# Performance work log

Hardware: AMD Instinct MI355X
Metric: run time of the kernel (lower is better)

## Reference

```python
import jax, jax.numpy as jnp
import numpy as np

B, C_IN, N = 64, 1, 8192
WIDTH, MODES, NLAYERS = 64, 16, 4


def setup_inputs() -> dict:
    key = jax.random.key(0)
    ks = jax.random.split(key, 10)
    scale = 1.0 / (WIDTH * WIDTH)
    inp = {
        "x": jax.random.normal(ks[0], (B, C_IN, N), dtype=jnp.float32),
        # lifting p: Linear(2, width)
        "p_w": jax.random.normal(ks[1], (WIDTH, 2), dtype=jnp.float32) * 0.5,
        "p_b": jax.random.normal(ks[2], (WIDTH,), dtype=jnp.float32) * 0.1,
        # 4 spectral conv weights, complex stored as real/imag (uniform like torch.rand cfloat)
        "sc_wr": scale * jax.random.uniform(ks[3], (NLAYERS, WIDTH, WIDTH, MODES), dtype=jnp.float32),
        "sc_wi": scale * jax.random.uniform(ks[4], (NLAYERS, WIDTH, WIDTH, MODES), dtype=jnp.float32),
        # 4 pointwise (1x1) conv weights/biases
        "w_w": jax.random.normal(ks[5], (NLAYERS, WIDTH, WIDTH), dtype=jnp.float32) / np.sqrt(WIDTH),
        "w_b": jax.random.normal(ks[6], (NLAYERS, WIDTH), dtype=jnp.float32) * 0.1,
        # projection q: Linear(width, 1)
        "q_w": jax.random.normal(ks[7], (1, WIDTH), dtype=jnp.float32) / np.sqrt(WIDTH),
        "q_b": jax.random.normal(ks[8], (1,), dtype=jnp.float32) * 0.1,
    }
    return inp


def spectral_conv(x, wr, wi, n):
    # x: [b, i, n] real; weights complex [i, o, modes]
    x_ft = jnp.fft.rfft(x, axis=-1)                      # [b, i, n//2+1] complex
    w = (wr + 1j * wi).astype(jnp.complex64)
    out_modes = jnp.einsum('bix,iox->box', x_ft[:, :, :MODES], w)
    out_ft = jnp.zeros((x.shape[0], w.shape[1], n // 2 + 1), dtype=jnp.complex64)
    out_ft = out_ft.at[:, :, :MODES].set(out_modes)
    return jnp.fft.irfft(out_ft, n=n, axis=-1)


def reference(x, p_w, p_b, sc_wr, sc_wi, w_w, w_b, q_w, q_b):
    b, _, n = x.shape
    grid = jnp.broadcast_to(jnp.linspace(0.0, 1.0, n, dtype=jnp.float32)[None, None, :], (b, 1, n))
    h = jnp.concatenate([x, grid], axis=1)               # [b, 2, n]
    # lifting: Linear over channel dim
    h = jnp.einsum('bcn,wc->bwn', h, p_w) + p_b[None, :, None]
    for l in range(NLAYERS):
        x1 = spectral_conv(h, sc_wr[l], sc_wi[l], n)
        x2 = jnp.einsum('bin,oi->bon', h, w_w[l]) + w_b[l][None, :, None]
        h = jax.nn.gelu(x1 + x2, approximate=False)
    out = jnp.einsum('bwn,ow->bon', h, q_w) + q_b[None, :, None]  # [b, 1, n]
    return out
```

## Files before the change

kernel.cpp:

```cpp
#include <hip/hip_runtime.h>
#include <math.h>


typedef _Float16 f16;
typedef _Float16 f16x2 __attribute__((ext_vector_type(2)));
typedef _Float16 f16x4 __attribute__((ext_vector_type(4)));
typedef _Float16 f16x8 __attribute__((ext_vector_type(8)));
typedef float    f32x2 __attribute__((ext_vector_type(2)));
typedef float    f32x4 __attribute__((ext_vector_type(4)));
typedef unsigned int u32;

#define BB 64
#define NN 8192

#define HT_S 64
#define HO_S 136
#define WS_S 72
#define MS_S 40
#define BI_S 40
#define BF_S 136

__device__ __forceinline__ int ht_swz(int n) { return ((n & 7) ^ ((n >> 3) & 7)) << 3; }

__device__ __forceinline__ float gelu_f(float v) {
    float x  = v * 0.70710678118654752f;
    float ax = fabsf(x);
    float t  = __builtin_amdgcn_rcpf(fmaf(0.3275911f, ax, 1.0f));
    float p  = fmaf(1.061405429f, t, -1.453152027f);
    p = fmaf(p, t, 1.421413741f);
    p = fmaf(p, t, -0.284496736f);
    p = fmaf(p, t, 0.254829592f);
    p = p * t;
    float e  = __expf(-x * x);
    float er = fmaf(-p, e, 1.0f);
    er = copysignf(er, x);
    return 0.5f * fmaf(v, er, v);
}

__global__ __launch_bounds__(256) void fill_basis(f16* __restrict__ basF,
                                                  f16* __restrict__ basI,
                                                  const float* __restrict__ w_w,
                                                  f16* __restrict__ Wh,
                                                  float* __restrict__ Sz) {
    int n = blockIdx.x * 256 + threadIdx.x;
    f16 row[32];
#pragma unroll
    for (int k = 0; k < 16; ++k) {
        float s, c;
        sincospif((float)(k * n) * (1.0f / 4096.0f), &s, &c);
        basF[k * NN + n]        = (f16)c;
        basF[(16 + k) * NN + n] = (f16)(-s);
        row[2 * k]     = (f16)c;
        row[2 * k + 1] = (f16)s;
    }
#pragma unroll
    for (int q = 0; q < 4; ++q) *(f16x8*)&basI[n * 32 + 8 * q] = *(f16x8*)&row[8 * q];
    Wh[n]        = (f16)w_w[n];
    Wh[n + 8192] = (f16)w_w[n + 8192];
    f32x4* S4 = (f32x4*)Sz;
    f32x4 z = {0.f, 0.f, 0.f, 0.f};
#pragma unroll
    for (int u = 0; u < 4; ++u) S4[n * 4 + u] = z;
}

__global__ __launch_bounds__(1024) void mode_mix(float* __restrict__ S,
                                                 const float* __restrict__ wr,
                                                 const float* __restrict__ wi,
                                                 f16* __restrict__ Mph) {
    int b = blockIdx.x, t = threadIdx.x;
    __shared__ float Ss[32 * 66];
    if (t < 512) {
        f32x4 v = *(const f32x4*)&S[b * 2048 + t * 4];
        int rw = t >> 4, cl = (t & 15) * 4;
#pragma unroll
        for (int e = 0; e < 4; ++e) Ss[rw * 66 + cl + e] = v[e];
    }
    __syncthreads();
    *(f32x2*)&S[b * 2048 + t * 2] = (f32x2){0.f, 0.f};

    int o = t >> 4, k = t & 15;
    const float* wrp = wr + o * 16 + k;
    const float* wip = wi + o * 16 + k;
    float ar = 0.f, ai = 0.f;
#pragma unroll 8
    for (int i = 0; i < 64; ++i) {
        float sr = Ss[k * 66 + i], si = Ss[(16 + k) * 66 + i];
        float wrv = wrp[i * 1024];
        float wiv = wip[i * 1024];
        ar = fmaf(sr, wrv, ar); ar = fmaf(-si, wiv, ar);
        ai = fmaf(sr, wiv, ai); ai = fmaf(si, wrv, ai);
    }
    float sc = (k == 0 ? 1.0f : 2.0f) * (1.0f / 8192.0f);
    f16x2 outv = { (f16)(sc * ar), (f16)(-sc * ai) };
    *(f16x2*)&Mph[b * 2048 + o * 32 + 2 * k] = outv;
}

__device__ __forceinline__ void dft_epilogue(const f16* Hout, const f16* BasF,
                                             float* __restrict__ S, int b,
                                             int lane, int wv) {
    int q = lane >> 4, l15 = lane & 15;
    f32x4 sacc[2] = {{0.f,0.f,0.f,0.f},{0.f,0.f,0.f,0.f}};
#pragma unroll
    for (int ks = 0; ks < 4; ++ks) {
        int o = (wv << 4) + l15;
        f16x8 bh = *(const f16x8*)&Hout[o * HO_S + ks * 32 + q * 8];
#pragma unroll
        for (int mt = 0; mt < 2; ++mt) {
            f16x8 af = *(const f16x8*)&BasF[(mt * 16 + l15) * BF_S + ks * 32 + q * 8];
            sacc[mt] = __builtin_amdgcn_mfma_f32_16x16x32_f16(af, bh, sacc[mt], 0, 0, 0);
        }
    }
#pragma unroll
    for (int mt = 0; mt < 2; ++mt)
#pragma unroll
        for (int r = 0; r < 4; ++r)
            atomicAdd(&S[(b * 32 + mt * 16 + q * 4 + r) * 64 + (wv << 4) + l15],
                      sacc[mt][r]);
}

__global__ __launch_bounds__(256, 3) void lift_kernel(const float* __restrict__ x,
                                                      const float* __restrict__ p_w,
                                                      const float* __restrict__ p_b,
                                                      f16* __restrict__ h,
                                                      const f16* __restrict__ basF_g,
                                                      float* __restrict__ S) {
    __shared__ f16 Hout[64 * HO_S];
    __shared__ f16 BasF[32 * BF_S];
    int t = threadIdx.x;
    int b = blockIdx.x >> 6;
    int n0 = (blockIdx.x & 63) << 7;
#pragma unroll
    for (int r = 0; r < 4; ++r) {
        int o = (t >> 4) + 16 * r;
        int ns = (t & 15) << 3;
        float w0 = p_w[2 * o], w1 = p_w[2 * o + 1], pb = p_b[o];
        f16 vals[8];
#pragma unroll
        for (int j = 0; j < 8; ++j) {
            int n = n0 + ns + j;
            float xv = x[(b << 13) + n];
            vals[j] = (f16)(w0 * xv + w1 * ((float)n * (1.0f / 8191.0f)) + pb);
        }
        *(f16x8*)&Hout[o * HO_S + ns] = *(f16x8*)vals;
        *(f16x8*)(h + (((size_t)(b * 64 + o)) << 13) + n0 + ns) = *(f16x8*)vals;
    }
#pragma unroll
    for (int u = 0; u < 2; ++u) {
        int km = t >> 3, nn = (t & 7) * 16 + u * 8;
        *(f16x8*)&BasF[km * BF_S + nn] = *(const f16x8*)&basF_g[km * NN + n0 + nn];
    }
    __syncthreads();
    dft_epilogue(Hout, BasF, S, b, t & 63, t >> 6);
}

template <int DO_DFT>
__global__ __launch_bounds__(256, 3) void layer_kernel(f16* __restrict__ h,
                                                       const f16* __restrict__ Wl_h,
                                                       const float* __restrict__ bl,
                                                       const f16* __restrict__ Mph,
                                                       const f16* __restrict__ basF_g,
                                                       const f16* __restrict__ basI_g,
                                                       float* __restrict__ S,
                                                       const float* __restrict__ q_w,
                                                       const float* __restrict__ q_b,
                                                       float* __restrict__ out) {
    __shared__ __align__(16) char pool[16384 + 9216];
    f16* Ht   = (f16*)pool;
    f16* Ws   = (f16*)(pool + 16384);
    f16* Hout = (f16*)pool;
    __shared__ f16 Ms2[64 * MS_S];
    __shared__ f16 BasI[128 * BI_S];
    __shared__ f16 BasF[32 * BF_S];
    __shared__ float bls[64];
    int t = threadIdx.x;
    int b = blockIdx.x >> 6;
    int n0 = (blockIdx.x & 63) << 7;
    f16* hb = h + (((size_t)(b * 64)) << 13) + n0;

    if (t < 128) {
        int ig = t >> 4, nb = t & 15;
        int i0 = ig << 3, ns = nb << 3;
        f16x8 R[8];
#pragma unroll
        for (int k = 0; k < 8; ++k)
            R[k] = *(const f16x8*)(hb + ((size_t)(i0 + k) << 13) + ns);
        const u32* rd = (const u32*)R;
        int swz = nb & 7;
#pragma unroll
        for (int j = 0; j < 8; ++j) {
            u32 o[4] __attribute__((aligned(16)));
            u32 sel = (j & 1) ? 0x07060302u : 0x05040100u;
            int jd = j >> 1;
#pragma unroll
            for (int e = 0; e < 4; ++e)
                o[e] = __builtin_amdgcn_perm(rd[(2 * e + 1) * 4 + jd],
                                             rd[(2 * e) * 4 + jd], sel);
            int col = i0 ^ ((j ^ swz) << 3);
            *(f16x8*)&Ht[(ns + j) * HT_S + col] = *(const f16x8*)o;
        }
    } else {
        int t2 = t - 128;
        {
            int o = t2 & 63, hs = (t2 >> 6) * 32;
            const f16* src = Wl_h + o * 64 + hs;
            f16* dst = &Ws[o * WS_S + hs];
#pragma unroll
            for (int u = 0; u < 4; ++u) *(f16x8*)&dst[8 * u] = *(const f16x8*)&src[8 * u];
        }
        {
            int o = t2 >> 1, seg = (t2 & 1) * 16;
            const f16* src = Mph + b * 2048 + o * 32 + seg;
            f16* dst = &Ms2[o * MS_S + seg];
            *(f16x8*)&dst[0] = *(const f16x8*)&src[0];
            *(f16x8*)&dst[8] = *(const f16x8*)&src[8];
        }
        {
            const f16* src = basI_g + (size_t)(n0 + t2) * 32;
            f16* dst = &BasI[t2 * BI_S];
#pragma unroll
            for (int u = 0; u < 4; ++u) *(f16x8*)&dst[8 * u] = *(const f16x8*)&src[8 * u];
        }
        if (DO_DFT) {
            int km = t2 >> 2, seg = (t2 & 3) * 32;
            const f16* src = basF_g + km * NN + n0 + seg;
            f16* dst = &BasF[km * BF_S + seg];
#pragma unroll
            for (int u = 0; u < 4; ++u) *(f16x8*)&dst[8 * u] = *(const f16x8*)&src[8 * u];
        }
    }
    if (t < 64) bls[t] = bl[t];
    __syncthreads();

    int lane = t & 63, wv = t >> 6;
    int q = lane >> 4, l15 = lane & 15;

    f16x8 Bw[4][2], Bm[4];
#pragma unroll
    for (int ct = 0; ct < 4; ++ct) {
#pragma unroll
        for (int ks = 0; ks < 2; ++ks)
            Bw[ct][ks] = *(const f16x8*)&Ws[(ct * 16 + l15) * WS_S + ks * 32 + q * 8];
        Bm[ct] = *(const f16x8*)&Ms2[(ct * 16 + l15) * MS_S + q * 8];
    }

    f32x4 acc[4][2];
#pragma unroll
    for (int ct = 0; ct < 4; ++ct)
#pragma unroll
        for (int m = 0; m < 2; ++m) acc[ct][m] = (f32x4){0.f, 0.f, 0.f, 0.f};

#pragma unroll
    for (int mtl = 0; mtl < 2; ++mtl) {
        int nrow = (2 * wv + mtl) * 16 + l15;
        const f16* hrow = &Ht[nrow * HT_S];
        int g3 = ht_swz(nrow);
#pragma unroll
        for (int ks = 0; ks < 2; ++ks) {
            f16x8 Ah = *(const f16x8*)&hrow[(ks * 32 + q * 8) ^ g3];
#pragma unroll
            for (int ct = 0; ct < 4; ++ct)
                acc[ct][mtl] = __builtin_amdgcn_mfma_f32_16x16x32_f16(
                    Ah, Bw[ct][ks], acc[ct][mtl], 0, 0, 0);
        }
        f16x8 Ab = *(const f16x8*)&BasI[nrow * BI_S + q * 8];
#pragma unroll
        for (int ct = 0; ct < 4; ++ct)
            acc[ct][mtl] = __builtin_amdgcn_mfma_f32_16x16x32_f16(
                Ab, Bm[ct], acc[ct][mtl], 0, 0, 0);
    }

    float bv[4];
#pragma unroll
    for (int ct = 0; ct < 4; ++ct) bv[ct] = bls[ct * 16 + l15];
    __syncthreads();
#pragma unroll
    for (int ct = 0; ct < 4; ++ct) {
        int o = ct * 16 + l15;
#pragma unroll
        for (int mtl = 0; mtl < 2; ++mtl) {
            int nbase = (2 * wv + mtl) * 16 + q * 4;
            float g[4];
#pragma unroll
            for (int r = 0; r < 4; ++r)
                g[r] = gelu_f(acc[ct][mtl][r] + bv[ct]);
            f16x2 lo = __builtin_bit_cast(f16x2, __builtin_amdgcn_cvt_pkrtz(g[0], g[1]));
            f16x2 hi = __builtin_bit_cast(f16x2, __builtin_amdgcn_cvt_pkrtz(g[2], g[3]));
            f16x4 pk = {lo[0], lo[1], hi[0], hi[1]};
            *(f16x4*)&Hout[o * HO_S + nbase] = pk;
        }
    }
    __syncthreads();

    if (DO_DFT) {
        dft_epilogue(Hout, BasF, S, b, lane, wv);
#pragma unroll
        for (int r = 0; r < 4; ++r) {
            int o = (t >> 4) + 16 * r;
            int ns = (t & 15) << 3;
            *(f16x8*)(hb + ((size_t)o << 13) + ns) = *(f16x8*)&Hout[o * HO_S + ns];
        }
    } else {
        if (t < 128) {
            int n = t;
            float s = q_b[0];
#pragma unroll 8
            for (int o = 0; o < 64; ++o) s += q_w[o] * (float)Hout[o * HO_S + n];
            out[(b << 13) + n0 + n] = s;
        }
    }
}

extern "C" void kernel_launch(void* const* d_in, const int* in_sizes, int n_in,
                              void* d_out, int out_size, void* d_ws, size_t ws_size,
                              hipStream_t stream) {
    const float* x     = (const float*)d_in[0];
    const float* p_w   = (const float*)d_in[1];
    const float* p_b   = (const float*)d_in[2];
    const float* sc_wr = (const float*)d_in[3];
    const float* sc_wi = (const float*)d_in[4];
    const float* w_w   = (const float*)d_in[5];
    const float* w_b   = (const float*)d_in[6];
    const float* q_w   = (const float*)d_in[7];
    const float* q_b   = (const float*)d_in[8];
    float* out = (float*)d_out;

    char* ws = (char*)d_ws;
    f16*   h    = (f16*)ws;
    float* S    = (float*)(ws + 67108864ull);
    f16*   Mph  = (f16*)(ws + 67633152ull);
    f16*   basF = (f16*)(ws + 67895296ull);
    f16*   basI = (f16*)(ws + 68419584ull);
    f16*   Wh   = (f16*)(ws + 68943872ull);

    hipLaunchKernelGGL(fill_basis, dim3(NN / 256), dim3(256), 0, stream,
                       basF, basI, w_w, Wh, S);
    hipLaunchKernelGGL(lift_kernel, dim3(BB * 64), dim3(256), 0, stream,
                       x, p_w, p_b, h, basF, S);
    for (int l = 0; l < 4; ++l) {
        hipLaunchKernelGGL(mode_mix, dim3(BB), dim3(1024), 0, stream,
                           S, sc_wr + l * 65536, sc_wi + l * 65536, Mph);
        if (l < 3) {
            hipLaunchKernelGGL((layer_kernel<1>), dim3(BB * 64), dim3(256), 0, stream,
                               h, Wh + l * 4096, w_b + l * 64, Mph, basF, basI, S,
                               q_w, q_b, out);
        } else {
            hipLaunchKernelGGL((layer_kernel<0>), dim3(BB * 64), dim3(256), 0, stream,
                               h, Wh + l * 4096, w_b + l * 64, Mph, basF, basI, S,
                               q_w, q_b, out);
        }
    }
}
```

Baseline: 277.5 us.

## Split forward DFT into a standalone kernel and process two tiles per layer block

The per-tile DFT epilogue with global float atomics is moved into a dedicated dft_kernel that reads h from global memory and reduces across waves in shared memory, so S no longer needs zeroing or atomics. Layer blocks now handle two 128-column tiles each, loading weights once and raising the occupancy hint. The final layer folds the q projection into registers with shuffle reductions instead of staging in LDS. The trade-off is an extra kernel launch and an extra full read of h per layer in exchange for removing atomic contention and the BasF staging.

```diff
diff --git a/kernel.cpp b/kernel.cpp
--- a/kernel.cpp
+++ b/kernel.cpp
@@ -6,7 +6,6 @@
 typedef _Float16 f16x2 __attribute__((ext_vector_type(2)));
 typedef _Float16 f16x4 __attribute__((ext_vector_type(4)));
 typedef _Float16 f16x8 __attribute__((ext_vector_type(8)));
-typedef float    f32x2 __attribute__((ext_vector_type(2)));
 typedef float    f32x4 __attribute__((ext_vector_type(4)));
 typedef unsigned int u32;
 
@@ -16,9 +15,8 @@
 #define HT_S 64
 #define HO_S 136
 #define WS_S 72
-#define MS_S 40
+#define MS_S 32
 #define BI_S 40
-#define BF_S 136
 
 __device__ __forceinline__ int ht_swz(int n) { return ((n & 7) ^ ((n >> 3) & 7)) << 3; }
 
@@ -40,8 +38,7 @@
 __global__ __launch_bounds__(256) void fill_basis(f16* __restrict__ basF,
                                                   f16* __restrict__ basI,
                                                   const float* __restrict__ w_w,
-                                                  f16* __restrict__ Wh,
-                                                  float* __restrict__ Sz) {
+                                                  f16* __restrict__ Wh) {
     int n = blockIdx.x * 256 + threadIdx.x;
     f16 row[32];
 #pragma unroll
@@ -57,13 +54,71 @@
     for (int q = 0; q < 4; ++q) *(f16x8*)&basI[n * 32 + 8 * q] = *(f16x8*)&row[8 * q];
     Wh[n]        = (f16)w_w[n];
     Wh[n + 8192] = (f16)w_w[n + 8192];
-    f32x4* S4 = (f32x4*)Sz;
-    f32x4 z = {0.f, 0.f, 0.f, 0.f};
-#pragma unroll
-    for (int u = 0; u < 4; ++u) S4[n * 4 + u] = z;
-}
-
-__global__ __launch_bounds__(1024) void mode_mix(float* __restrict__ S,
+}
+
+__global__ __launch_bounds__(256) void lift_kernel(const float* __restrict__ x,
+                                                   const float* __restrict__ p_w,
+                                                   const float* __restrict__ p_b,
+                                                   f16* __restrict__ h) {
+    int t = threadIdx.x;
+    int b = blockIdx.x >> 6;
+    int n0 = (blockIdx.x & 63) << 7;
+    int ns = (t & 15) << 3;
+    f32x4 X0 = *(const f32x4*)&x[(b << 13) + n0 + ns];
+    f32x4 X1 = *(const f32x4*)&x[(b << 13) + n0 + ns + 4];
+#pragma unroll
+    for (int r = 0; r < 4; ++r) {
+        int o = (t >> 4) + 16 * r;
+        float w0 = p_w[2 * o], w1 = p_w[2 * o + 1], pb = p_b[o];
+        f16 vals[8];
+#pragma unroll
+        for (int j = 0; j < 8; ++j) {
+            int n = n0 + ns + j;
+            float xv = (j < 4) ? X0[j] : X1[j - 4];
+            vals[j] = (f16)(w0 * xv + w1 * ((float)n * (1.0f / 8191.0f)) + pb);
+        }
+        *(f16x8*)(h + (((size_t)(b * 64 + o)) << 13) + n0 + ns) = *(f16x8*)vals;
+    }
+}
+
+__global__ __launch_bounds__(512) void dft_kernel(const f16* __restrict__ h,
+                                                  const f16* __restrict__ basF,
+                                                  float* __restrict__ S) {
+    __shared__ float Sp[8 * 512];
+    int b = blockIdx.x >> 2, ct = blockIdx.x & 3;
+    int t = threadIdx.x;
+    int wv = t >> 6, lane = t & 63;
+    int q = lane >> 4, l15 = lane & 15;
+
+    const f16* hrow = h + (((size_t)(b * 64 + ct * 16 + l15)) << 13);
+    const f16* a0 = basF + (size_t)l15 * NN;
+    const f16* a1 = basF + (size_t)(16 + l15) * NN;
+    int kb0 = (wv << 10) + (q << 3);
+
+    f32x4 acc0 = {0.f, 0.f, 0.f, 0.f}, acc1 = {0.f, 0.f, 0.f, 0.f};
+#pragma unroll 4
+    for (int kk = 0; kk < 32; ++kk) {
+        int kb = kb0 + (kk << 5);
+        f16x8 Bv = *(const f16x8*)&hrow[kb];
+        f16x8 A0 = *(const f16x8*)&a0[kb];
+        f16x8 A1 = *(const f16x8*)&a1[kb];
+        acc0 = __builtin_amdgcn_mfma_f32_16x16x32_f16(A0, Bv, acc0, 0, 0, 0);
+        acc1 = __builtin_amdgcn_mfma_f32_16x16x32_f16(A1, Bv, acc1, 0, 0, 0);
+    }
+#pragma unroll
+    for (int r = 0; r < 4; ++r) {
+        Sp[wv * 512 + (q * 4 + r) * 16 + l15]       = acc0[r];
+        Sp[wv * 512 + (16 + q * 4 + r) * 16 + l15]  = acc1[r];
+    }
+    __syncthreads();
+    float s = 0.f;
+#pragma unroll
+    for (int w = 0; w < 8; ++w) s += Sp[w * 512 + t];
+    int km = t >> 4, il = t & 15;
+    S[(b * 32 + km) * 64 + ct * 16 + il] = s;
+}
+
+__global__ __launch_bounds__(1024) void mode_mix(const float* __restrict__ S,
                                                  const float* __restrict__ wr,
                                                  const float* __restrict__ wi,
                                                  f16* __restrict__ Mph) {
@@ -76,8 +131,6 @@
         for (int e = 0; e < 4; ++e) Ss[rw * 66 + cl + e] = v[e];
     }
     __syncthreads();
-    *(f32x2*)&S[b * 2048 + t * 2] = (f32x2){0.f, 0.f};
-
     int o = t >> 4, k = t & 15;
     const float* wrp = wr + o * 16 + k;
     const float* wip = wi + o * 16 + k;
@@ -95,72 +148,12 @@
     *(f16x2*)&Mph[b * 2048 + o * 32 + 2 * k] = outv;
 }
 
-__device__ __forceinline__ void dft_epilogue(const f16* Hout, const f16* BasF,
-                                             float* __restrict__ S, int b,
-                                             int lane, int wv) {
-    int q = lane >> 4, l15 = lane & 15;
-    f32x4 sacc[2] = {{0.f,0.f,0.f,0.f},{0.f,0.f,0.f,0.f}};
-#pragma unroll
-    for (int ks = 0; ks < 4; ++ks) {
-        int o = (wv << 4) + l15;
-        f16x8 bh = *(const f16x8*)&Hout[o * HO_S + ks * 32 + q * 8];
-#pragma unroll
-        for (int mt = 0; mt < 2; ++mt) {
-            f16x8 af = *(const f16x8*)&BasF[(mt * 16 + l15) * BF_S + ks * 32 + q * 8];
-            sacc[mt] = __builtin_amdgcn_mfma_f32_16x16x32_f16(af, bh, sacc[mt], 0, 0, 0);
-        }
-    }
-#pragma unroll
-    for (int mt = 0; mt < 2; ++mt)
-#pragma unroll
-        for (int r = 0; r < 4; ++r)
-            atomicAdd(&S[(b * 32 + mt * 16 + q * 4 + r) * 64 + (wv << 4) + l15],
-                      sacc[mt][r]);
-}
-
-__global__ __launch_bounds__(256, 3) void lift_kernel(const float* __restrict__ x,
-                                                      const float* __restrict__ p_w,
-                                                      const float* __restrict__ p_b,
-                                                      f16* __restrict__ h,
-                                                      const f16* __restrict__ basF_g,
-                                                      float* __restrict__ S) {
-    __shared__ f16 Hout[64 * HO_S];
-    __shared__ f16 BasF[32 * BF_S];
-    int t = threadIdx.x;
-    int b = blockIdx.x >> 6;
-    int n0 = (blockIdx.x & 63) << 7;
-#pragma unroll
-    for (int r = 0; r < 4; ++r) {
-        int o = (t >> 4) + 16 * r;
-        int ns = (t & 15) << 3;
-        float w0 = p_w[2 * o], w1 = p_w[2 * o + 1], pb = p_b[o];
-        f16 vals[8];
-#pragma unroll
-        for (int j = 0; j < 8; ++j) {
-            int n = n0 + ns + j;
-            float xv = x[(b << 13) + n];
-            vals[j] = (f16)(w0 * xv + w1 * ((float)n * (1.0f / 8191.0f)) + pb);
-        }
-        *(f16x8*)&Hout[o * HO_S + ns] = *(f16x8*)vals;
-        *(f16x8*)(h + (((size_t)(b * 64 + o)) << 13) + n0 + ns) = *(f16x8*)vals;
-    }
-#pragma unroll
-    for (int u = 0; u < 2; ++u) {
-        int km = t >> 3, nn = (t & 7) * 16 + u * 8;
-        *(f16x8*)&BasF[km * BF_S + nn] = *(const f16x8*)&basF_g[km * NN + n0 + nn];
-    }
-    __syncthreads();
-    dft_epilogue(Hout, BasF, S, b, t & 63, t >> 6);
-}
-
-template <int DO_DFT>
-__global__ __launch_bounds__(256, 3) void layer_kernel(f16* __restrict__ h,
+template <int PROJ>
+__global__ __launch_bounds__(256, 4) void layer_kernel(f16* __restrict__ h,
                                                        const f16* __restrict__ Wl_h,
                                                        const float* __restrict__ bl,
                                                        const f16* __restrict__ Mph,
-                                                       const f16* __restrict__ basF_g,
                                                        const f16* __restrict__ basI_g,
-                                                       float* __restrict__ S,
                                                        const float* __restrict__ q_w,
                                                        const float* __restrict__ q_b,
                                                        float* __restrict__ out) {
@@ -170,35 +163,14 @@
     f16* Hout = (f16*)pool;
     __shared__ f16 Ms2[64 * MS_S];
     __shared__ f16 BasI[128 * BI_S];
-    __shared__ f16 BasF[32 * BF_S];
-    __shared__ float bls[64];
     int t = threadIdx.x;
-    int b = blockIdx.x >> 6;
-    int n0 = (blockIdx.x & 63) << 7;
-    f16* hb = h + (((size_t)(b * 64)) << 13) + n0;
-
-    if (t < 128) {
-        int ig = t >> 4, nb = t & 15;
-        int i0 = ig << 3, ns = nb << 3;
-        f16x8 R[8];
-#pragma unroll
-        for (int k = 0; k < 8; ++k)
-            R[k] = *(const f16x8*)(hb + ((size_t)(i0 + k) << 13) + ns);
-        const u32* rd = (const u32*)R;
-        int swz = nb & 7;
-#pragma unroll
-        for (int j = 0; j < 8; ++j) {
-            u32 o[4] __attribute__((aligned(16)));
-            u32 sel = (j & 1) ? 0x07060302u : 0x05040100u;
-            int jd = j >> 1;
-#pragma unroll
-            for (int e = 0; e < 4; ++e)
-                o[e] = __builtin_amdgcn_perm(rd[(2 * e + 1) * 4 + jd],
-                                             rd[(2 * e) * 4 + jd], sel);
-            int col = i0 ^ ((j ^ swz) << 3);
-            *(f16x8*)&Ht[(ns + j) * HT_S + col] = *(const f16x8*)o;
-        }
-    } else {
+    int b = blockIdx.x >> 5;
+    int g = blockIdx.x & 31;
+    f16* hbase = h + (((size_t)(b * 64)) << 13);
+    int lane = t & 63, wv = t >> 6;
+    int q = lane >> 4, l15 = lane & 15;
+
+    if (t >= 128) {
         int t2 = t - 128;
         {
             int o = t2 & 63, hs = (t2 >> 6) * 32;
@@ -214,99 +186,135 @@
             *(f16x8*)&dst[0] = *(const f16x8*)&src[0];
             *(f16x8*)&dst[8] = *(const f16x8*)&src[8];
         }
-        {
+    }
+    float bv[4];
+#pragma unroll
+    for (int ct = 0; ct < 4; ++ct) bv[ct] = bl[ct * 16 + l15];
+
+    f16x8 Bw[4][2], Bm[4];
+
+    for (int tile = 0; tile < 2; ++tile) {
+        int n0 = ((g << 1) + tile) << 7;
+        f16* hbt = hbase + n0;
+
+        if (t < 128) {
+            int ig = t >> 4, nb = t & 15;
+            int i0 = ig << 3, ns = nb << 3;
+            f16x8 R[8];
+#pragma unroll
+            for (int k = 0; k < 8; ++k)
+                R[k] = *(const f16x8*)(hbt + ((size_t)(i0 + k) << 13) + ns);
+            const u32* rd = (const u32*)R;
+            int swz = nb & 7;
+#pragma unroll
+            for (int j = 0; j < 8; ++j) {
+                u32 o[4] __attribute__((aligned(16)));
+                u32 sel = (j & 1) ? 0x07060302u : 0x05040100u;
+                int jd = j >> 1;
+#pragma unroll
+                for (int e = 0; e < 4; ++e)
+                    o[e] = __builtin_amdgcn_perm(rd[(2 * e + 1) * 4 + jd],
+                                                 rd[(2 * e) * 4 + jd], sel);
+                int col = i0 ^ ((j ^ swz) << 3);
+                *(f16x8*)&Ht[(ns + j) * HT_S + col] = *(const f16x8*)o;
+            }
+        } else {
+            int t2 = t - 128;
             const f16* src = basI_g + (size_t)(n0 + t2) * 32;
             f16* dst = &BasI[t2 * BI_S];
 #pragma unroll
             for (int u = 0; u < 4; ++u) *(f16x8*)&dst[8 * u] = *(const f16x8*)&src[8 * u];
         }
-        if (DO_DFT) {
-            int km = t2 >> 2, seg = (t2 & 3) * 32;
-            const f16* src = basF_g + km * NN + n0 + seg;
-            f16* dst = &BasF[km * BF_S + seg];
-#pragma unroll
-            for (int u = 0; u < 4; ++u) *(f16x8*)&dst[8 * u] = *(const f16x8*)&src[8 * u];
-        }
-    }
-    if (t < 64) bls[t] = bl[t];
-    __syncthreads();
-
-    int lane = t & 63, wv = t >> 6;
-    int q = lane >> 4, l15 = lane & 15;
-
-    f16x8 Bw[4][2], Bm[4];
-#pragma unroll
-    for (int ct = 0; ct < 4; ++ct) {
-#pragma unroll
-        for (int ks = 0; ks < 2; ++ks)
-            Bw[ct][ks] = *(const f16x8*)&Ws[(ct * 16 + l15) * WS_S + ks * 32 + q * 8];
-        Bm[ct] = *(const f16x8*)&Ms2[(ct * 16 + l15) * MS_S + q * 8];
-    }
-
-    f32x4 acc[4][2];
-#pragma unroll
-    for (int ct = 0; ct < 4; ++ct)
-#pragma unroll
-        for (int m = 0; m < 2; ++m) acc[ct][m] = (f32x4){0.f, 0.f, 0.f, 0.f};
-
-#pragma unroll
-    for (int mtl = 0; mtl < 2; ++mtl) {
-        int nrow = (2 * wv + mtl) * 16 + l15;
-        const f16* hrow = &Ht[nrow * HT_S];
-        int g3 = ht_swz(nrow);
-#pragma unroll
-        for (int ks = 0; ks < 2; ++ks) {
-            f16x8 Ah = *(const f16x8*)&hrow[(ks * 32 + q * 8) ^ g3];
+        __syncthreads();
+
+        if (tile == 0) {
+#pragma unroll
+            for (int ct = 0; ct < 4; ++ct) {
+#pragma unroll
+                for (int ks = 0; ks < 2; ++ks)
+                    Bw[ct][ks] = *(const f16x8*)&Ws[(ct * 16 + l15) * WS_S + ks * 32 + q * 8];
+                Bm[ct] = *(const f16x8*)&Ms2[(ct * 16 + l15) * MS_S + q * 8];
+            }
+        }
+
+        f32x4 acc[4][2];
+#pragma unroll
+        for (int ct = 0; ct < 4; ++ct)
+#pragma unroll
+            for (int m = 0; m < 2; ++m) acc[ct][m] = (f32x4){0.f, 0.f, 0.f, 0.f};
+
+#pragma unroll
+        for (int mtl = 0; mtl < 2; ++mtl) {
+            int nrow = (2 * wv + mtl) * 16 + l15;
+            const f16* hrow = &Ht[nrow * HT_S];
+            int g3 = ht_swz(nrow);
+#pragma unroll
+            for (int ks = 0; ks < 2; ++ks) {
+                f16x8 Ah = *(const f16x8*)&hrow[(ks * 32 + q * 8) ^ g3];
+#pragma unroll
+                for (int ct = 0; ct < 4; ++ct)
+                    acc[ct][mtl] = __builtin_amdgcn_mfma_f32_16x16x32_f16(
+                        Ah, Bw[ct][ks], acc[ct][mtl], 0, 0, 0);
+            }
+            f16x8 Ab = *(const f16x8*)&BasI[nrow * BI_S + q * 8];
 #pragma unroll
             for (int ct = 0; ct < 4; ++ct)
                 acc[ct][mtl] = __builtin_amdgcn_mfma_f32_16x16x32_f16(
-                    Ah, Bw[ct][ks], acc[ct][mtl], 0, 0, 0);
-        }
-        f16x8 Ab = *(const f16x8*)&BasI[nrow * BI_S + q * 8];
-#pragma unroll
-        for (int ct = 0; ct < 4; ++ct)
-            acc[ct][mtl] = __builtin_amdgcn_mfma_f32_16x16x32_f16(
-                Ab, Bm[ct], acc[ct][mtl], 0, 0, 0);
-    }
-
-    float bv[4];
-#pragma unroll
-    for (int ct = 0; ct < 4; ++ct) bv[ct] = bls[ct * 16 + l15];
-    __syncthreads();
-#pragma unroll
-    for (int ct = 0; ct < 4; ++ct) {
-        int o = ct * 16 + l15;
-#pragma unroll
-        for (int mtl = 0; mtl < 2; ++mtl) {
-            int nbase = (2 * wv + mtl) * 16 + q * 4;
-            float g[4];
-#pragma unroll
-            for (int r = 0; r < 4; ++r)
-                g[r] = gelu_f(acc[ct][mtl][r] + bv[ct]);
-            f16x2 lo = __builtin_bit_cast(f16x2, __builtin_amdgcn_cvt_pkrtz(g[0], g[1]));
-            f16x2 hi = __builtin_bit_cast(f16x2, __builtin_amdgcn_cvt_pkrtz(g[2], g[3]));
-            f16x4 pk = {lo[0], lo[1], hi[0], hi[1]};
-            *(f16x4*)&Hout[o * HO_S + nbase] = pk;
-        }
-    }
-    __syncthreads();
-
-    if (DO_DFT) {
-        dft_epilogue(Hout, BasF, S, b, lane, wv);
-#pragma unroll
-        for (int r = 0; r < 4; ++r) {
-            int o = (t >> 4) + 16 * r;
-            int ns = (t & 15) << 3;
-            *(f16x8*)(hb + ((size_t)o << 13) + ns) = *(f16x8*)&Hout[o * HO_S + ns];
-        }
-    } else {
-        if (t < 128) {
-            int n = t;
-            float s = q_b[0];
-#pragma unroll 8
-            for (int o = 0; o < 64; ++o) s += q_w[o] * (float)Hout[o * HO_S + n];
-            out[(b << 13) + n0 + n] = s;
-        }
+                    Ab, Bm[ct], acc[ct][mtl], 0, 0, 0);
+        }
+
+        if (!PROJ) {
+            __syncthreads();
+#pragma unroll
+            for (int ct = 0; ct < 4; ++ct) {
+                int o = ct * 16 + l15;
+#pragma unroll
+                for (int mtl = 0; mtl < 2; ++mtl) {
+                    int nbase = (2 * wv + mtl) * 16 + q * 4;
+                    float gg[4];
+#pragma unroll
+                    for (int r = 0; r < 4; ++r)
+                        gg[r] = gelu_f(acc[ct][mtl][r] + bv[ct]);
+                    f16x2 lo = __builtin_bit_cast(f16x2, __builtin_amdgcn_cvt_pkrtz(gg[0], gg[1]));
+                    f16x2 hi = __builtin_bit_cast(f16x2, __builtin_amdgcn_cvt_pkrtz(gg[2], gg[3]));
+                    f16x4 pk = {lo[0], lo[1], hi[0], hi[1]};
+                    *(f16x4*)&Hout[o * HO_S + nbase] = pk;
+                }
+            }
+            __syncthreads();
+#pragma unroll
+            for (int r = 0; r < 4; ++r) {
+                int o = (t >> 4) + 16 * r;
+                int ns2 = (t & 15) << 3;
+                *(f16x8*)(hbt + ((size_t)o << 13) + ns2) = *(f16x8*)&Hout[o * HO_S + ns2];
+            }
+        } else {
+            float qv[4];
+#pragma unroll
+            for (int ct = 0; ct < 4; ++ct) qv[ct] = q_w[ct * 16 + l15];
+            float part[2][4] = {{0.f,0.f,0.f,0.f},{0.f,0.f,0.f,0.f}};
+#pragma unroll
+            for (int ct = 0; ct < 4; ++ct)
+#pragma unroll
+                for (int mtl = 0; mtl < 2; ++mtl)
+#pragma unroll
+                    for (int r = 0; r < 4; ++r)
+                        part[mtl][r] = fmaf(qv[ct],
+                            gelu_f(acc[ct][mtl][r] + bv[ct]), part[mtl][r]);
+#pragma unroll
+            for (int mtl = 0; mtl < 2; ++mtl)
+#pragma unroll
+                for (int r = 0; r < 4; ++r) {
+                    float s = part[mtl][r];
+#pragma unroll
+                    for (int m = 1; m < 16; m <<= 1)
+                        s += __shfl_xor(s, m, 64);
+                    if (l15 == 0)
+                        out[(b << 13) + n0 + (2 * wv + mtl) * 16 + q * 4 + r] =
+                            s + q_b[0];
+                }
+        }
+        if (tile == 0) __syncthreads();
     }
 }
 
@@ -333,19 +341,21 @@
     f16*   Wh   = (f16*)(ws + 68943872ull);
 
     hipLaunchKernelGGL(fill_basis, dim3(NN / 256), dim3(256), 0, stream,
-                       basF, basI, w_w, Wh, S);
+                       basF, basI, w_w, Wh);
     hipLaunchKernelGGL(lift_kernel, dim3(BB * 64), dim3(256), 0, stream,
-                       x, p_w, p_b, h, basF, S);
+                       x, p_w, p_b, h);
     for (int l = 0; l < 4; ++l) {
+        hipLaunchKernelGGL(dft_kernel, dim3(BB * 4), dim3(512), 0, stream,
+                           h, basF, S);
         hipLaunchKernelGGL(mode_mix, dim3(BB), dim3(1024), 0, stream,
                            S, sc_wr + l * 65536, sc_wi + l * 65536, Mph);
         if (l < 3) {
-            hipLaunchKernelGGL((layer_kernel<1>), dim3(BB * 64), dim3(256), 0, stream,
-                               h, Wh + l * 4096, w_b + l * 64, Mph, basF, basI, S,
+            hipLaunchKernelGGL((layer_kernel<0>), dim3(BB * 32), dim3(256), 0, stream,
+                               h, Wh + l * 4096, w_b + l * 64, Mph, basI,
                                q_w, q_b, out);
         } else {
-            hipLaunchKernelGGL((layer_kernel<0>), dim3(BB * 64), dim3(256), 0, stream,
-                               h, Wh + l * 4096, w_b + l * 64, Mph, basF, basI, S,
+            hipLaunchKernelGGL((layer_kernel<1>), dim3(BB * 32), dim3(256), 0, stream,
+                               h, Wh + l * 4096, w_b + l * 64, Mph, basI,
                                q_w, q_b, out);
         }
     }
```

Measured after the change: 352.7 us. +27.1%, slower.
